# Kernel optimization log

Measured on AMD Instinct MI355X. Metric: run time of the kernel, lower is better.

## Reference

```python
import jax, jax.numpy as jnp
import numpy as np

B, S, H, NH = 2, 2048, 1024, 16
HD = H // NH  # 64
SCALE = HD ** -0.5


def setup_inputs() -> dict:
    key = jax.random.key(0)
    k1, k2, k3 = jax.random.split(key, 3)
    x = jax.random.normal(k1, (B, S, H), dtype=jnp.float32)
    w_qkv = jax.random.normal(k2, (H, 3 * H), dtype=jnp.float32) * (H ** -0.5)
    b_qkv = jnp.zeros((3 * H,), dtype=jnp.float32)
    w_out = jax.random.normal(k3, (H, H), dtype=jnp.float32) * (H ** -0.5)
    b_out = jnp.zeros((H,), dtype=jnp.float32)
    return {"x": x, "w_qkv": w_qkv, "b_qkv": b_qkv, "w_out": w_out, "b_out": b_out}


def reference(x, w_qkv, b_qkv, w_out, b_out):
    # qkv projection: [B,S,3H] -> split -> [B,NH,S,HD] each
    qkv = x @ w_qkv + b_qkv
    q, k, v = jnp.split(qkv, 3, axis=-1)
    def heads(t):
        return t.reshape(B, S, NH, HD).transpose(0, 2, 1, 3)  # [B,NH,S,HD]
    q, k, v = heads(q), heads(k), heads(v)
    # full (non-causal) softmax attention; chunking in the original is
    # math-equivalent since each query row attends over all keys
    scores = jnp.einsum('bhqd,bhkd->bhqk', q, k) * SCALE
    attn = jax.nn.softmax(scores, axis=-1)
    out = jnp.einsum('bhqk,bhkd->bhqd', attn, v)  # [B,NH,S,HD]
    out = out.transpose(0, 2, 1, 3).reshape(B, S, H)
    # to_out linear (Dropout is identity in eval mode)
    return out @ w_out + b_out
```

## Files before the change

### kernel.cpp

```cpp
#include <hip/hip_runtime.h>
#include <cstdint>

using u16 = unsigned short;
typedef __bf16 bf16x8 __attribute__((ext_vector_type(8)));
typedef __bf16 bf16x4 __attribute__((ext_vector_type(4)));
typedef __bf16 bf16x2 __attribute__((ext_vector_type(2)));
typedef float f32x4 __attribute__((ext_vector_type(4)));

#define MFMA16(a, b, c) __builtin_amdgcn_mfma_f32_16x16x32_bf16((a), (b), (c), 0, 0, 0)

__device__ __forceinline__ u16 f2bf(float f) {
  union { float f; uint32_t u; } c; c.f = f;
  uint32_t u = c.u;
  u += 0x7fffu + ((u >> 16) & 1u);
  return (u16)(u >> 16);
}

#if __has_builtin(__builtin_amdgcn_global_load_lds)
#define GLOAD_LDS16(g, l)                                                      \
  __builtin_amdgcn_global_load_lds(                                            \
      (__attribute__((address_space(1))) void*)(g),                            \
      (__attribute__((address_space(3))) void*)(l), 16, 0, 0)
#else
#define GLOAD_LDS16(g, l) do { *(uint4*)(l) = *(const uint4*)(g); } while (0)
#endif

__device__ __forceinline__ bf16x8 ptrans(const f32x4 lo, const f32x4 hi) {
  union W { bf16x2 h; uint32_t u; } wl0, wl1, wh0, wh1;
  wl0.h[0] = (__bf16)lo[0]; wl0.h[1] = (__bf16)lo[1];
  wl1.h[0] = (__bf16)lo[2]; wl1.h[1] = (__bf16)lo[3];
  wh0.h[0] = (__bf16)hi[0]; wh0.h[1] = (__bf16)hi[1];
  wh1.h[0] = (__bf16)hi[2]; wh1.h[1] = (__bf16)hi[3];
  uint32_t a0 = wl0.u, b0 = wh0.u, a1 = wl1.u, b1 = wh1.u;
  asm("v_permlane32_swap_b32 %0, %1" : "+v"(a0), "+v"(b0));
  asm("v_permlane16_swap_b32 %0, %1" : "+v"(a0), "+v"(b0));
  asm("v_permlane32_swap_b32 %0, %1" : "+v"(a1), "+v"(b1));
  asm("v_permlane16_swap_b32 %0, %1" : "+v"(a1), "+v"(b1));
  union R { uint32_t u[4]; bf16x8 v; } r;
  r.u[0] = a0; r.u[1] = a1; r.u[2] = b0; r.u[3] = b1;
  return r.v;
}

__global__ __launch_bounds__(256) void prep(
    const float* __restrict__ x, const float* __restrict__ w_qkv,
    const float* __restrict__ w_out, u16* __restrict__ xb,
    u16* __restrict__ wqT, u16* __restrict__ woT) {
  const int bid = blockIdx.x, tid = threadIdx.x;
  if (bid < 4096) {
    int i = (bid * 256 + tid) * 4;
    float4 v = *(const float4*)&x[i];
    ushort4 p;
    p.x = f2bf(v.x); p.y = f2bf(v.y); p.z = f2bf(v.z); p.w = f2bf(v.w);
    *(ushort4*)&xb[i] = p;
    return;
  }
  __shared__ float tile[32][33];
  int t = bid - 4096;
  const float* in;
  u16* outp;
  int C, bx, by;
  if (t < 3072) { in = w_qkv; outp = wqT; C = 3072; bx = (t % 96) * 32; by = (t / 96) * 32; }
  else { t -= 3072; in = w_out; outp = woT; C = 1024; bx = (t % 32) * 32; by = (t / 32) * 32; }
  const int tx = tid & 31, ty = tid >> 5;
#pragma unroll
  for (int r2 = 0; r2 < 4; ++r2)
    tile[ty + r2 * 8][tx] = in[(size_t)(by + ty + r2 * 8) * C + bx + tx];
  __syncthreads();
#pragma unroll
  for (int r2 = 0; r2 < 4; ++r2)
    outp[(size_t)(bx + ty + r2 * 8) * 1024 + by + tx] = f2bf(tile[tx][ty + r2 * 8]);
}

__global__ __launch_bounds__(256, 3) void gemm_qkv(
    const u16* __restrict__ A, const u16* __restrict__ Bt,
    const float* __restrict__ bias,
    u16* __restrict__ qb, u16* __restrict__ kb, u16* __restrict__ vb,
    int M, int N, int K) {
  __shared__ u16 As[128 * 32];
  __shared__ u16 Bs[128 * 32];
  const int tid = threadIdx.x;
  const int m0 = blockIdx.x * 128;
  const int n0 = blockIdx.y * 128;
  const int lane = tid & 63, w = tid >> 6;
  const int quad = lane >> 4, l16 = lane & 15;
  const int wr = w >> 1, wc = w & 1;

  f32x4 acc[4][4] = {};

  const int r0 = tid >> 2, p0 = tid & 3;
  const int r1 = r0 + 64;
  const int c8 = p0 ^ ((r0 >> 1) & 3);
  const u16* ga0 = A + (size_t)(m0 + r0) * K + c8 * 8;
  const u16* ga1 = A + (size_t)(m0 + r1) * K + c8 * 8;
  const u16* gb0 = Bt + (size_t)(n0 + r0) * K + c8 * 8;
  const u16* gb1 = Bt + (size_t)(n0 + r1) * K + c8 * 8;
  u16* la0 = &As[tid * 8];
  u16* la1 = &As[(tid + 256) * 8];
  u16* lb0 = &Bs[tid * 8];
  u16* lb1 = &Bs[(tid + 256) * 8];

  int aoff[4], boff[4];
#pragma unroll
  for (int i = 0; i < 4; ++i) {
    int ra = wr * 64 + i * 16 + l16;
    aoff[i] = (ra * 4 + (quad ^ ((ra >> 1) & 3))) * 8;
    int rb = wc * 64 + i * 16 + l16;
    boff[i] = (rb * 4 + (quad ^ ((rb >> 1) & 3))) * 8;
  }

  const int nIter = K >> 5;
  for (int kt = 0; kt < nIter; ++kt) {
    __syncthreads();
    const int kk = kt << 5;
    GLOAD_LDS16(ga0 + kk, la0);
    GLOAD_LDS16(ga1 + kk, la1);
    GLOAD_LDS16(gb0 + kk, lb0);
    GLOAD_LDS16(gb1 + kk, lb1);
    __syncthreads();
    bf16x8 af[4], bfr[4];
#pragma unroll
    for (int i = 0; i < 4; ++i) af[i] = *(const bf16x8*)&As[aoff[i]];
#pragma unroll
    for (int j = 0; j < 4; ++j) bfr[j] = *(const bf16x8*)&Bs[boff[j]];
#pragma unroll
    for (int i = 0; i < 4; ++i)
#pragma unroll
      for (int j = 0; j < 4; ++j)
        acc[i][j] = MFMA16(af[i], bfr[j], acc[i][j]);
  }

  const int S = 2048, NH = 16;
#pragma unroll
  for (int i = 0; i < 4; ++i) {
    const int mb = m0 + wr * 64 + i * 16 + quad * 4;
#pragma unroll
    for (int j = 0; j < 4; ++j) {
      const int n = n0 + wc * 64 + j * 16 + l16;
      const float bv = bias[n];
      const int which = n >> 10;
      const int hn = n & 1023;
      const int h = hn >> 6, d = hn & 63;
      const int b = mb >> 11, s = mb & 2047;
      const int bh = b * NH + h;
      if (which == 2) {
        ushort4 pk;
        pk.x = f2bf(acc[i][j][0] + bv);
        pk.y = f2bf(acc[i][j][1] + bv);
        pk.z = f2bf(acc[i][j][2] + bv);
        pk.w = f2bf(acc[i][j][3] + bv);
        *(ushort4*)&vb[((size_t)bh * 64 + d) * S + s] = pk;
      } else {
        const float sc = (which == 0) ? 0.18033688f : 1.0f;
        u16* dst = (which == 0) ? qb : kb;
#pragma unroll
        for (int r = 0; r < 4; ++r)
          dst[((size_t)bh * S + s + r) * 64 + d] = f2bf((acc[i][j][r] + bv) * sc);
      }
    }
  }
}

__global__ __launch_bounds__(256, 2) void gemm_out(
    const u16* __restrict__ A, const u16* __restrict__ Bt,
    const float* __restrict__ bias, float* __restrict__ outf,
    int M, int N, int K) {
  __shared__ u16 As[64 * 32];
  __shared__ u16 Bs[128 * 32];
  const int tid = threadIdx.x;
  const int m0 = blockIdx.x * 64;
  const int n0 = blockIdx.y * 128;
  const int lane = tid & 63, w = tid >> 6;
  const int quad = lane >> 4, l16 = lane & 15;
  const int wr = w >> 1, wc = w & 1;

  f32x4 acc[2][4] = {};

  const int r0 = tid >> 2, p0 = tid & 3;
  const int c8 = p0 ^ ((r0 >> 1) & 3);
  const u16* ga0 = A + (size_t)(m0 + r0) * K + c8 * 8;
  const u16* gb0 = Bt + (size_t)(n0 + r0) * K + c8 * 8;
  const u16* gb1 = Bt + (size_t)(n0 + r0 + 64) * K + c8 * 8;
  u16* la0 = &As[tid * 8];
  u16* lb0 = &Bs[tid * 8];
  u16* lb1 = &Bs[(tid + 256) * 8];

  int aoff[2], boff[4];
#pragma unroll
  for (int i = 0; i < 2; ++i) {
    int ra = wr * 32 + i * 16 + l16;
    aoff[i] = (ra * 4 + (quad ^ ((ra >> 1) & 3))) * 8;
  }
#pragma unroll
  for (int j = 0; j < 4; ++j) {
    int rb = wc * 64 + j * 16 + l16;
    boff[j] = (rb * 4 + (quad ^ ((rb >> 1) & 3))) * 8;
  }

  const int nIter = K >> 5;
  for (int kt = 0; kt < nIter; ++kt) {
    __syncthreads();
    const int kk = kt << 5;
    GLOAD_LDS16(ga0 + kk, la0);
    GLOAD_LDS16(gb0 + kk, lb0);
    GLOAD_LDS16(gb1 + kk, lb1);
    __syncthreads();
    bf16x8 af[2], bfr[4];
#pragma unroll
    for (int i = 0; i < 2; ++i) af[i] = *(const bf16x8*)&As[aoff[i]];
#pragma unroll
    for (int j = 0; j < 4; ++j) bfr[j] = *(const bf16x8*)&Bs[boff[j]];
#pragma unroll
    for (int i = 0; i < 2; ++i)
#pragma unroll
      for (int j = 0; j < 4; ++j)
        acc[i][j] = MFMA16(af[i], bfr[j], acc[i][j]);
  }

#pragma unroll
  for (int i = 0; i < 2; ++i) {
    const int mb = m0 + wr * 32 + i * 16 + quad * 4;
#pragma unroll
    for (int j = 0; j < 4; ++j) {
      const int n = n0 + wc * 64 + j * 16 + l16;
      const float bv = bias[n];
#pragma unroll
      for (int r = 0; r < 4; ++r)
        outf[(size_t)(mb + r) * N + n] = acc[i][j][r] + bv;
    }
  }
}

__global__ __launch_bounds__(256, 2) void attn_fa(
    const u16* __restrict__ qg, const u16* __restrict__ kg,
    const u16* __restrict__ vg, u16* __restrict__ o) {
  const int S = 2048;
  const int lin = blockIdx.x;
  const int xcd = lin & 7, chunk = lin >> 3;
  const int bh = xcd * 4 + (chunk & 3);
  const int qblk = chunk >> 2;
  const int b = bh >> 4, h = bh & 15;
  const int tid = threadIdx.x, w = tid >> 6, lane = tid & 63;
  const int quad = lane >> 4, l16 = lane & 15;

  __shared__ u16 Ks[2][8192];
  __shared__ u16 Vs[2][8192];

  const int q0 = qblk * 128 + w * 32;
  const u16* qp = qg + ((size_t)bh * S + q0 + l16) * 64 + quad * 8;
  const bf16x8 qf00 = *(const bf16x8*)qp;
  const bf16x8 qf01 = *(const bf16x8*)(qp + 32);
  const bf16x8 qf10 = *(const bf16x8*)(qp + 1024);
  const bf16x8 qf11 = *(const bf16x8*)(qp + 1024 + 32);

  f32x4 accO0[4] = {}, accO1[4] = {};
  f32x4 accL0 = {}, accL1 = {};

  bf16x8 ones;
#pragma unroll
  for (int i = 0; i < 8; ++i) ones[i] = (__bf16)1.0f;

  const u16* kbase = kg + (size_t)bh * S * 64;
  const u16* vbase = vg + (size_t)bh * 64 * S;

  const int sr0 = tid >> 3, sp0 = tid & 7;
  const int c8s = sp0 ^ (sr0 & 7);
  const u16* kSrc = kbase + (size_t)sr0 * 64 + c8s * 8;
  const int vd0 = tid >> 3, vg0 = tid & 7;
  const u16* vSrc = vbase + (size_t)vd0 * S + (vg0 ^ (vd0 & 7)) * 8;

  const int kgA = (quad ^ (l16 & 7)) * 8;
  const int kgB = ((quad + 4) ^ (l16 & 7)) * 8;

#pragma unroll
  for (int seg = 0; seg < 4; ++seg) {
    GLOAD_LDS16(kSrc + (size_t)seg * 32 * 64, &Ks[0][(seg * 256 + tid) * 8]);
    GLOAD_LDS16(vSrc + (size_t)(seg & 1) * 32 * S + (seg >> 1) * 64,
                &Vs[0][(seg * 256 + tid) * 8]);
  }

  for (int kt = 0; kt < 16; ++kt) {
    const int cur = kt & 1;
    __syncthreads();
    const u16* Kc = Ks[cur];
    const u16* Vc = Vs[cur];

    bf16x8 kf00[4], kf01[4], kf10[4], kf11[4];
    bf16x8 vf00[4], vf01[4], vf10[4], vf11[4];
#pragma unroll
    for (int ct = 0; ct < 4; ++ct) {
      const int rb0 = (ct * 16 + l16) * 64;
      const int rb1 = (64 + ct * 16 + l16) * 64;
      kf00[ct] = *(const bf16x8*)&Kc[rb0 + kgA];
      kf01[ct] = *(const bf16x8*)&Kc[rb0 + kgB];
      kf10[ct] = *(const bf16x8*)&Kc[rb1 + kgA];
      kf11[ct] = *(const bf16x8*)&Kc[rb1 + kgB];
      vf00[ct] = *(const bf16x8*)&Vc[rb0 + kgA];
      vf01[ct] = *(const bf16x8*)&Vc[rb0 + kgB];
      vf10[ct] = *(const bf16x8*)&Vc[4096 + rb0 + kgA];
      vf11[ct] = *(const bf16x8*)&Vc[4096 + rb0 + kgB];
    }

    if (kt + 1 < 16) {
      const int nb = cur ^ 1;
#pragma unroll
      for (int seg = 0; seg < 4; ++seg) {
        GLOAD_LDS16(kSrc + (size_t)((kt + 1) * 128 + seg * 32) * 64,
                    &Ks[nb][(seg * 256 + tid) * 8]);
        GLOAD_LDS16(vSrc + (size_t)(seg & 1) * 32 * S + (kt + 1) * 128 +
                        (seg >> 1) * 64,
                    &Vs[nb][(seg * 256 + tid) * 8]);
      }
    }

    f32x4 s0[4] = {}, s1[4] = {}, t0[4] = {}, t1[4] = {};
    __builtin_amdgcn_s_setprio(1);
#pragma unroll
    for (int ct = 0; ct < 4; ++ct) {
      s0[ct] = MFMA16(kf00[ct], qf00, s0[ct]);
      s0[ct] = MFMA16(kf01[ct], qf01, s0[ct]);
      s1[ct] = MFMA16(kf00[ct], qf10, s1[ct]);
      s1[ct] = MFMA16(kf01[ct], qf11, s1[ct]);
      t0[ct] = MFMA16(kf10[ct], qf00, t0[ct]);
      t0[ct] = MFMA16(kf11[ct], qf01, t0[ct]);
      t1[ct] = MFMA16(kf10[ct], qf10, t1[ct]);
      t1[ct] = MFMA16(kf11[ct], qf11, t1[ct]);
    }
    __builtin_amdgcn_s_setprio(0);

#pragma unroll
    for (int ct = 0; ct < 4; ++ct)
#pragma unroll
      for (int r = 0; r < 4; ++r) {
        s0[ct][r] = __builtin_amdgcn_exp2f(s0[ct][r]);
        s1[ct][r] = __builtin_amdgcn_exp2f(s1[ct][r]);
        t0[ct][r] = __builtin_amdgcn_exp2f(t0[ct][r]);
        t1[ct][r] = __builtin_amdgcn_exp2f(t1[ct][r]);
      }

    bf16x8 pf00 = ptrans(s0[0], s0[1]);
    bf16x8 pf01 = ptrans(s0[2], s0[3]);
    bf16x8 pf10 = ptrans(s1[0], s1[1]);
    bf16x8 pf11 = ptrans(s1[2], s1[3]);
    bf16x8 pg00 = ptrans(t0[0], t0[1]);
    bf16x8 pg01 = ptrans(t0[2], t0[3]);
    bf16x8 pg10 = ptrans(t1[0], t1[1]);
    bf16x8 pg11 = ptrans(t1[2], t1[3]);

    __builtin_amdgcn_s_setprio(1);
    accL0 = MFMA16(ones, pf00, accL0);
    accL0 = MFMA16(ones, pf01, accL0);
    accL1 = MFMA16(ones, pf10, accL1);
    accL1 = MFMA16(ones, pf11, accL1);
    accL0 = MFMA16(ones, pg00, accL0);
    accL0 = MFMA16(ones, pg01, accL0);
    accL1 = MFMA16(ones, pg10, accL1);
    accL1 = MFMA16(ones, pg11, accL1);
#pragma unroll
    for (int ct = 0; ct < 4; ++ct) {
      accO0[ct] = MFMA16(vf00[ct], pf00, accO0[ct]);
      accO0[ct] = MFMA16(vf01[ct], pf01, accO0[ct]);
      accO1[ct] = MFMA16(vf00[ct], pf10, accO1[ct]);
      accO1[ct] = MFMA16(vf01[ct], pf11, accO1[ct]);
      accO0[ct] = MFMA16(vf10[ct], pg00, accO0[ct]);
      accO0[ct] = MFMA16(vf11[ct], pg01, accO0[ct]);
      accO1[ct] = MFMA16(vf10[ct], pg10, accO1[ct]);
      accO1[ct] = MFMA16(vf11[ct], pg11, accO1[ct]);
    }
    __builtin_amdgcn_s_setprio(0);
  }

  const float inv0 = 1.f / accL0[0], inv1 = 1.f / accL1[0];

  const int s0r = q0 + l16, s1r = q0 + 16 + l16;
#pragma unroll
  for (int ct = 0; ct < 4; ++ct) {
    ushort4 pk;
    pk.x = f2bf(accO0[ct][0] * inv0);
    pk.y = f2bf(accO0[ct][1] * inv0);
    pk.z = f2bf(accO0[ct][2] * inv0);
    pk.w = f2bf(accO0[ct][3] * inv0);
    *(ushort4*)&o[(size_t)(b * S + s0r) * 1024 + h * 64 + ct * 16 + quad * 4] = pk;
    pk.x = f2bf(accO1[ct][0] * inv1);
    pk.y = f2bf(accO1[ct][1] * inv1);
    pk.z = f2bf(accO1[ct][2] * inv1);
    pk.w = f2bf(accO1[ct][3] * inv1);
    *(ushort4*)&o[(size_t)(b * S + s1r) * 1024 + h * 64 + ct * 16 + quad * 4] = pk;
  }
}


extern "C" void kernel_launch(void* const* d_in, const int* in_sizes, int n_in,
                              void* d_out, int out_size, void* d_ws, size_t ws_size,
                              hipStream_t stream) {
  const float* x = (const float*)d_in[0];
  const float* w_qkv = (const float*)d_in[1];
  const float* b_qkv = (const float*)d_in[2];
  const float* w_out = (const float*)d_in[3];
  const float* b_out = (const float*)d_in[4];
  float* out = (float*)d_out;

  u16* xb = (u16*)d_ws;
  u16* wqT = xb + 4096 * 1024;
  u16* woT = wqT + 3072 * 1024;
  u16* qb = woT + 1024 * 1024;
  u16* kb = qb + 4194304;
  u16* vb = kb + 4194304;
  u16* ao = vb + 4194304;

  prep<<<8192, 256, 0, stream>>>(x, w_qkv, w_out, xb, wqT, woT);
  gemm_qkv<<<dim3(32, 24), 256, 0, stream>>>(xb, wqT, b_qkv, qb, kb, vb,
                                             4096, 3072, 1024);
  attn_fa<<<512, 256, 0, stream>>>(qb, kb, vb, ao);
  gemm_out<<<dim3(64, 8), 256, 0, stream>>>(ao, woT, b_out, out,
                                            4096, 1024, 1024);
}
```

Baseline: 172.7 us.

## Fuse x fp32-to-bf16 conversion into QKV GEMM and remap blocks per XCD

Removes the separate pass that converts x to bf16. The QKV GEMM now streams fp32 x tiles straight into LDS with a swizzled layout and converts them to bf16 while loading the MFMA fragments. This saves writing and re-reading the bf16 copy of x, at the cost of twice the LDS and global traffic for A inside the GEMM, plus conversion ALU work on every k-step. The GEMM also remaps block IDs so that each XCD handles a contiguous group of M tiles, which should improve L2 reuse. The attention K/V staging is moved into a macro with no change in behaviour.

```diff
diff --git a/kernel.cpp b/kernel.cpp
--- a/kernel.cpp
+++ b/kernel.cpp
@@ -42,20 +42,11 @@
 }
 
 __global__ __launch_bounds__(256) void prep(
-    const float* __restrict__ x, const float* __restrict__ w_qkv,
-    const float* __restrict__ w_out, u16* __restrict__ xb,
+    const float* __restrict__ w_qkv, const float* __restrict__ w_out,
     u16* __restrict__ wqT, u16* __restrict__ woT) {
-  const int bid = blockIdx.x, tid = threadIdx.x;
-  if (bid < 4096) {
-    int i = (bid * 256 + tid) * 4;
-    float4 v = *(const float4*)&x[i];
-    ushort4 p;
-    p.x = f2bf(v.x); p.y = f2bf(v.y); p.z = f2bf(v.z); p.w = f2bf(v.w);
-    *(ushort4*)&xb[i] = p;
-    return;
-  }
+  const int tid = threadIdx.x;
   __shared__ float tile[32][33];
-  int t = bid - 4096;
+  int t = blockIdx.x;
   const float* in;
   u16* outp;
   int C, bx, by;
@@ -72,38 +63,41 @@
 }
 
 __global__ __launch_bounds__(256, 3) void gemm_qkv(
-    const u16* __restrict__ A, const u16* __restrict__ Bt,
+    const float* __restrict__ X, const u16* __restrict__ Bt,
     const float* __restrict__ bias,
     u16* __restrict__ qb, u16* __restrict__ kb, u16* __restrict__ vb,
     int M, int N, int K) {
-  __shared__ u16 As[128 * 32];
+  __shared__ float As4[128 * 32];
   __shared__ u16 Bs[128 * 32];
   const int tid = threadIdx.x;
-  const int m0 = blockIdx.x * 128;
-  const int n0 = blockIdx.y * 128;
+  const int lin = blockIdx.y * 32 + blockIdx.x;
+  const int xcd = lin & 7;
+  const int rr = lin >> 3;
+  const int mi = rr & 3, nj = rr >> 2;
+  const int m0 = (xcd * 4 + mi) * 128;
+  const int n0 = nj * 128;
   const int lane = tid & 63, w = tid >> 6;
   const int quad = lane >> 4, l16 = lane & 15;
   const int wr = w >> 1, wc = w & 1;
 
   f32x4 acc[4][4] = {};
 
+  const int tr = tid >> 3, tp = tid & 7;
+  const int ag = tp ^ (tr & 7);
+  const float* gaX = X + (size_t)(m0 + tr) * K + ag * 4;
+
   const int r0 = tid >> 2, p0 = tid & 3;
-  const int r1 = r0 + 64;
   const int c8 = p0 ^ ((r0 >> 1) & 3);
-  const u16* ga0 = A + (size_t)(m0 + r0) * K + c8 * 8;
-  const u16* ga1 = A + (size_t)(m0 + r1) * K + c8 * 8;
   const u16* gb0 = Bt + (size_t)(n0 + r0) * K + c8 * 8;
-  const u16* gb1 = Bt + (size_t)(n0 + r1) * K + c8 * 8;
-  u16* la0 = &As[tid * 8];
-  u16* la1 = &As[(tid + 256) * 8];
+  const u16* gb1 = Bt + (size_t)(n0 + r0 + 64) * K + c8 * 8;
   u16* lb0 = &Bs[tid * 8];
   u16* lb1 = &Bs[(tid + 256) * 8];
 
-  int aoff[4], boff[4];
+  int aoffA[4], boff[4];
 #pragma unroll
   for (int i = 0; i < 4; ++i) {
     int ra = wr * 64 + i * 16 + l16;
-    aoff[i] = (ra * 4 + (quad ^ ((ra >> 1) & 3))) * 8;
+    aoffA[i] = (ra * 8 + ((quad * 2) ^ (ra & 7))) * 4;
     int rb = wc * 64 + i * 16 + l16;
     boff[i] = (rb * 4 + (quad ^ ((rb >> 1) & 3))) * 8;
   }
@@ -112,14 +106,22 @@
   for (int kt = 0; kt < nIter; ++kt) {
     __syncthreads();
     const int kk = kt << 5;
-    GLOAD_LDS16(ga0 + kk, la0);
-    GLOAD_LDS16(ga1 + kk, la1);
+#pragma unroll
+    for (int j = 0; j < 4; ++j)
+      GLOAD_LDS16(gaX + (size_t)j * 32 * K + kk, &As4[(j * 256 + tid) * 4]);
     GLOAD_LDS16(gb0 + kk, lb0);
     GLOAD_LDS16(gb1 + kk, lb1);
     __syncthreads();
     bf16x8 af[4], bfr[4];
 #pragma unroll
-    for (int i = 0; i < 4; ++i) af[i] = *(const bf16x8*)&As[aoff[i]];
+    for (int i = 0; i < 4; ++i) {
+      f32x4 a0 = *(const f32x4*)&As4[aoffA[i]];
+      f32x4 a1 = *(const f32x4*)&As4[aoffA[i] ^ 4];
+      af[i][0] = (__bf16)a0[0]; af[i][1] = (__bf16)a0[1];
+      af[i][2] = (__bf16)a0[2]; af[i][3] = (__bf16)a0[3];
+      af[i][4] = (__bf16)a1[0]; af[i][5] = (__bf16)a1[1];
+      af[i][6] = (__bf16)a1[2]; af[i][7] = (__bf16)a1[3];
+    }
 #pragma unroll
     for (int j = 0; j < 4; ++j) bfr[j] = *(const bf16x8*)&Bs[boff[j]];
 #pragma unroll
@@ -153,8 +155,8 @@
         const float sc = (which == 0) ? 0.18033688f : 1.0f;
         u16* dst = (which == 0) ? qb : kb;
 #pragma unroll
-        for (int r = 0; r < 4; ++r)
-          dst[((size_t)bh * S + s + r) * 64 + d] = f2bf((acc[i][j][r] + bv) * sc);
+        for (int r2 = 0; r2 < 4; ++r2)
+          dst[((size_t)bh * S + s + r2) * 64 + d] = f2bf((acc[i][j][r2] + bv) * sc);
       }
     }
   }
@@ -265,18 +267,24 @@
   const int sr0 = tid >> 3, sp0 = tid & 7;
   const int c8s = sp0 ^ (sr0 & 7);
   const u16* kSrc = kbase + (size_t)sr0 * 64 + c8s * 8;
-  const int vd0 = tid >> 3, vg0 = tid & 7;
-  const u16* vSrc = vbase + (size_t)vd0 * S + (vg0 ^ (vd0 & 7)) * 8;
+  const u16* vSrc = vbase + (size_t)sr0 * S + c8s * 8;
 
   const int kgA = (quad ^ (l16 & 7)) * 8;
   const int kgB = ((quad + 4) ^ (l16 & 7)) * 8;
 
-#pragma unroll
-  for (int seg = 0; seg < 4; ++seg) {
-    GLOAD_LDS16(kSrc + (size_t)seg * 32 * 64, &Ks[0][(seg * 256 + tid) * 8]);
-    GLOAD_LDS16(vSrc + (size_t)(seg & 1) * 32 * S + (seg >> 1) * 64,
-                &Vs[0][(seg * 256 + tid) * 8]);
-  }
+#define STAGE_KV(KT, NB)                                                      \
+  {                                                                           \
+    _Pragma("unroll")                                                         \
+    for (int seg = 0; seg < 4; ++seg) {                                       \
+      GLOAD_LDS16(kSrc + (size_t)((KT) * 128 + seg * 32) * 64,                \
+                  &Ks[NB][(seg * 256 + tid) * 8]);                            \
+      GLOAD_LDS16(vSrc + (size_t)(seg & 1) * 32 * S + (KT) * 128 +            \
+                      (seg >> 1) * 64,                                        \
+                  &Vs[NB][(seg * 256 + tid) * 8]);                            \
+    }                                                                         \
+  }
+
+  STAGE_KV(0, 0);
 
   for (int kt = 0; kt < 16; ++kt) {
     const int cur = kt & 1;
@@ -300,17 +308,7 @@
       vf11[ct] = *(const bf16x8*)&Vc[4096 + rb0 + kgB];
     }
 
-    if (kt + 1 < 16) {
-      const int nb = cur ^ 1;
-#pragma unroll
-      for (int seg = 0; seg < 4; ++seg) {
-        GLOAD_LDS16(kSrc + (size_t)((kt + 1) * 128 + seg * 32) * 64,
-                    &Ks[nb][(seg * 256 + tid) * 8]);
-        GLOAD_LDS16(vSrc + (size_t)(seg & 1) * 32 * S + (kt + 1) * 128 +
-                        (seg >> 1) * 64,
-                    &Vs[nb][(seg * 256 + tid) * 8]);
-      }
-    }
+    if (kt + 1 < 16) STAGE_KV(kt + 1, cur ^ 1);
 
     f32x4 s0[4] = {}, s1[4] = {}, t0[4] = {}, t1[4] = {};
     __builtin_amdgcn_s_setprio(1);
@@ -368,6 +366,7 @@
     }
     __builtin_amdgcn_s_setprio(0);
   }
+#undef STAGE_KV
 
   const float inv0 = 1.f / accL0[0], inv1 = 1.f / accL1[0];
 
@@ -407,8 +406,8 @@
   u16* vb = kb + 4194304;
   u16* ao = vb + 4194304;
 
-  prep<<<8192, 256, 0, stream>>>(x, w_qkv, w_out, xb, wqT, woT);
-  gemm_qkv<<<dim3(32, 24), 256, 0, stream>>>(xb, wqT, b_qkv, qb, kb, vb,
+  prep<<<4096, 256, 0, stream>>>(w_qkv, w_out, wqT, woT);
+  gemm_qkv<<<dim3(32, 24), 256, 0, stream>>>(x, wqT, b_qkv, qb, kb, vb,
                                              4096, 3072, 1024);
   attn_fa<<<512, 256, 0, stream>>>(qb, kb, vb, ao);
   gemm_out<<<dim3(64, 8), 256, 0, stream>>>(ao, woT, b_out, out,
```

New measurement: 176.9 us. 1.02x slower.
